# Kernel tuning notes

Measured on AMD Instinct MI355X. Metric: run time of the kernel, lower is better.

Reference implementation:

```python
import jax, jax.numpy as jnp
import numpy as np

N_IND, N_ORG, N_EXT = 1_000_000, 300_000, 100_000
F = 64
E = 1_000_000
# (src_type, dst_type) per relation, in HeteroConv dict order:
# txn: ind->ind, org->ind, ext->ind, ind->org, org->org, ext->org; role: ind->org;
# rev_txn: ind->ind, org->ind, ext->ind, ind->org, org->org, ext->org; rev_role: org->ind
RELS = [("ind","ind"),("org","ind"),("ext","ind"),("ind","org"),("org","org"),("ext","org"),
        ("ind","org"),("ind","ind"),("org","ind"),("ext","ind"),("ind","org"),("org","org"),
        ("ext","org"),("org","ind")]
N_OF = {"ind": N_IND, "org": N_ORG, "ext": N_EXT}


def setup_inputs() -> dict:
    key = jax.random.key(0)
    ks = jax.random.split(key, 8)
    x_ind = jax.random.normal(ks[0], (N_IND, F), dtype=jnp.float32)
    x_org = jax.random.normal(ks[1], (N_ORG, F), dtype=jnp.float32)
    x_ext = jax.random.normal(ks[2], (N_EXT, F), dtype=jnp.float32)
    Wl = jax.random.normal(ks[3], (14, F, 1), dtype=jnp.float32) * 0.1
    Wr = jax.random.normal(ks[4], (14, F, 1), dtype=jnp.float32) * 0.1
    b = jax.random.normal(ks[5], (14, 1), dtype=jnp.float32) * 0.1
    # Per-relation edge_index with src/dst ids in the correct node-count ranges.
    eis = []
    for r, (s, d) in enumerate(RELS):
        k1, k2 = jax.random.split(jax.random.fold_in(ks[6], r))
        src = jax.random.randint(k1, (E,), 0, N_OF[s], dtype=jnp.int32)
        dst = jax.random.randint(k2, (E,), 0, N_OF[d], dtype=jnp.int32)
        eis.append(jnp.stack([src, dst]))
    edge_index = jnp.stack(eis)  # [14, 2, E]
    return {"x_ind": x_ind, "x_org": x_org, "x_ext": x_ext,
            "Wl": Wl, "Wr": Wr, "b": b, "edge_index": edge_index}


def _segment_mean(feat, dst, num_segments):
    # PyG 'mean' aggr: zero for isolated dst nodes.
    s = jax.ops.segment_sum(feat, dst, num_segments=num_segments)          # [N_dst, F]
    c = jax.ops.segment_sum(jnp.ones((dst.shape[0], 1), feat.dtype), dst,
                            num_segments=num_segments)                      # [N_dst, 1]
    return s / jnp.maximum(c, 1.0)


def reference(x_ind, x_org, x_ext, Wl, Wr, b, edge_index):
    x = {"ind": x_ind, "org": x_org, "ext": x_ext}
    out = {"ind": jnp.zeros((N_IND, 1), x_ind.dtype),
           "org": jnp.zeros((N_ORG, 1), x_org.dtype)}
    for r, (s, d) in enumerate(RELS):
        src, dst = edge_index[r, 0], edge_index[r, 1]
        agg = _segment_mean(x[s][src], dst, N_OF[d])   # mean of neighbor feats [N_dst, F]
        # SAGEConv: lin_l(agg) + lin_r(x_dst); bias lives in lin_l. HeteroConv sums relations.
        out[d] = out[d] + agg @ Wl[r] + x[d] @ Wr[r] + b[r]
    pred_ind = jax.nn.sigmoid(out["ind"])[:, 0]
    pred_org = jax.nn.sigmoid(out["org"])[:, 0]
    return (pred_ind, pred_org)
```

## Files before the change

kernel.cpp:

```cpp
#include <hip/hip_runtime.h>
#include <hip/hip_fp16.h>

#define N_IND 1000000
#define N_ORG 300000
#define N_EXT 100000
#define F 64
#define E_PER 1000000
#define NREL 14

#define BW 1024
#define NB_IND 977
#define NB_ORG 293
#define NBKT 1270
#define NB_H 1024
#define CHUNK 8192
#define COLS_PER_REL 123
#define NCOL (NREL * COLS_PER_REL)
#define LAST_N (E_PER - (COLS_PER_REL - 1) * CHUNK)
#define COLS_PER_TYPE (7 * COLS_PER_REL)
#define TSCAT 512

#define FIX_SCALE 262144.0f
#define FIX_INV   3.814697265625e-6f

static const size_t OFF_PAY      = 0;
static const size_t OFF_CNTOFF   = 14106624;
static const size_t OFF_CNTOFF_T = 15869952;
static const size_t OFF_P_IND    = 17633280;
static const size_t OFF_P_ORG    = 20133280;
static const size_t OFF_P_EXT    = 20883280;
static const size_t OFF_BASE_IND = 21083280;
static const size_t OFF_BASE_ORG = 22083280;
static const size_t OFF_WM_IND   = 22383280;
static const size_t OFF_WM_ORG   = 22383664;
static const size_t OFF_WM_EXT   = 22384048;
static const size_t OFF_BSUM     = 22384304;

__global__ void prep_kernel(const float* __restrict__ Wl,
                            const float* __restrict__ Wr,
                            const float* __restrict__ b,
                            float* __restrict__ wm_ind,
                            float* __restrict__ wm_org,
                            float* __restrict__ wm_ext,
                            float* __restrict__ bsum) {
    int t = threadIdx.x;
    const int ind_wl[5] = {0, 3, 6, 7, 10};
    const int org_wl[5] = {1, 4, 8, 11, 13};
    const int ext_wl[4] = {2, 5, 9, 12};
    const int ind_r[7]  = {0, 1, 2, 7, 8, 9, 13};
    const int org_r[7]  = {3, 4, 5, 6, 10, 11, 12};
#pragma unroll
    for (int k = 0; k < 5; ++k) wm_ind[k * 64 + t] = Wl[ind_wl[k] * 64 + t];
#pragma unroll
    for (int k = 0; k < 5; ++k) wm_org[k * 64 + t] = Wl[org_wl[k] * 64 + t];
#pragma unroll
    for (int k = 0; k < 4; ++k) wm_ext[k * 64 + t] = Wl[ext_wl[k] * 64 + t];
    float si = 0.f, so = 0.f;
#pragma unroll
    for (int k = 0; k < 7; ++k) {
        si += Wr[ind_r[k] * 64 + t];
        so += Wr[org_r[k] * 64 + t];
    }
    wm_ind[5 * 64 + t] = si;
    wm_org[5 * 64 + t] = so;
    if (t == 0) {
        float bi = 0.f, bo = 0.f;
#pragma unroll
        for (int k = 0; k < 7; ++k) { bi += b[ind_r[k]]; bo += b[org_r[k]]; }
        bsum[0] = bi;
        bsum[1] = bo;
    }
}

template <int K, bool HASBASE>
__global__ __launch_bounds__(256) void proj_kernel(
    const float* __restrict__ x, int n,
    const float* __restrict__ wm,
    __half* __restrict__ p,
    float* __restrict__ base_out,
    const float* __restrict__ bsum) {
    int i = blockIdx.x * 256 + threadIdx.x;
    if (i >= n) return;
    const float4* xv = (const float4*)(x + (size_t)i * F);
    float acc[K];
#pragma unroll
    for (int k = 0; k < K; ++k) acc[k] = 0.f;
#pragma unroll
    for (int c = 0; c < 16; ++c) {
        float4 v = xv[c];
#pragma unroll
        for (int k = 0; k < K; ++k) {
            const float* w = wm + k * 64 + c * 4;
            acc[k] += v.x * w[0] + v.y * w[1] + v.z * w[2] + v.w * w[3];
        }
    }
    constexpr int NP = HASBASE ? K - 1 : K;
#pragma unroll
    for (int k = 0; k < NP; ++k) p[(size_t)k * n + i] = __float2half_rn(acc[k]);
    if (HASBASE) base_out[i] = acc[K - 1] + bsum[0];
}

__global__ __launch_bounds__(TSCAT, 8) void scatter_kernel(
    const int* __restrict__ ei,
    const unsigned short* __restrict__ p_ind,
    const unsigned short* __restrict__ p_org,
    const unsigned short* __restrict__ p_ext,
    unsigned* __restrict__ pay,
    unsigned* __restrict__ cntoff) {
    const int srcType[NREL] = {0,1,2,0,1,2,0,0,1,2,0,1,2,1};
    const int srcSlot[NREL] = {0,0,0,1,1,1,2,3,2,2,4,3,3,4};
    const int dstSlot[NREL] = {0,1,2,0,1,2,3,3,4,5,4,5,6,6};

    __shared__ unsigned h[NB_H];
    __shared__ unsigned stage[CHUNK];
    __shared__ unsigned wsum[8];

    const int t = threadIdx.x;
    const int lane = t & 63, wv = t >> 6;

    const int cid = blockIdx.x;
    const int r = cid / COLS_PER_REL;
    const int i = cid - r * COLS_PER_REL;
    const int n = (i == COLS_PER_REL - 1) ? LAST_N : CHUNK;
    const int n4 = n >> 2;
    const int* srcp = ei + ((size_t)r * 2 + 0) * E_PER + (size_t)i * CHUNK;
    const int* dstp = ei + ((size_t)r * 2 + 1) * E_PER + (size_t)i * CHUNK;
    const unsigned slotbits = (unsigned)dstSlot[r] << 10;
    const int st = srcType[r];
    const unsigned short* psrc =
        (st == 0) ? p_ind + (size_t)srcSlot[r] * N_IND :
        (st == 1) ? p_org + (size_t)srcSlot[r] * N_ORG :
                    p_ext + (size_t)srcSlot[r] * N_EXT;

    h[t * 2 + 0] = 0u;
    h[t * 2 + 1] = 0u;
    __syncthreads();
    const int4* dst4 = (const int4*)dstp;
    int4 dreg[4];
#pragma unroll
    for (int u = 0; u < 4; ++u) {
        int k = t + u * TSCAT;
        if (k < n4) {
            int4 d = dst4[k];
            dreg[u] = d;
            atomicAdd(&h[d.x >> 10], 1u);
            atomicAdd(&h[d.y >> 10], 1u);
            atomicAdd(&h[d.z >> 10], 1u);
            atomicAdd(&h[d.w >> 10], 1u);
        }
    }
    __syncthreads();

    unsigned loc0 = h[t * 2 + 0], loc1 = h[t * 2 + 1];
    unsigned s0 = loc0 + loc1;
    unsigned x = s0;
#pragma unroll
    for (int d = 1; d < 64; d <<= 1) {
        unsigned v = __shfl_up(x, d, 64);
        if (lane >= d) x += v;
    }
    if (lane == 63) wsum[wv] = x;
    __syncthreads();
    unsigned base = x - s0;
    for (int j = 0; j < wv; ++j) base += wsum[j];
    unsigned* co = cntoff + (size_t)cid * NB_H;
    co[t * 2 + 0] = (base << 16) | loc0;
    h[t * 2 + 0] = base;
    base += loc0;
    co[t * 2 + 1] = (base << 16) | loc1;
    h[t * 2 + 1] = base;
    __syncthreads();

    const int4* src4 = (const int4*)srcp;
#pragma unroll
    for (int u = 0; u < 4; ++u) {
        int k = t + u * TSCAT;
        if (k < n4) {
            int4 s = src4[k];
            int4 d = dreg[u];
#pragma unroll
            for (int q = 0; q < 4; ++q) {
                int src = (q == 0) ? s.x : (q == 1) ? s.y : (q == 2) ? s.z : s.w;
                int dst = (q == 0) ? d.x : (q == 1) ? d.y : (q == 2) ? d.z : d.w;
                unsigned pvbits = psrc[src];
                unsigned word = (pvbits << 16) | slotbits | ((unsigned)dst & (BW - 1));
                unsigned pos = atomicAdd(&h[dst >> 10], 1u);
                stage[pos] = word;
            }
        }
    }
    __syncthreads();

    uint4* payc4 = (uint4*)(pay + (size_t)cid * CHUNK);
    const uint4* st4 = (const uint4*)stage;
    for (int k = t; k < n4; k += TSCAT) payc4[k] = st4[k];
}

__global__ __launch_bounds__(256) void transpose_kernel(
    const unsigned* __restrict__ in, unsigned* __restrict__ out) {
    __shared__ unsigned tb[32][33];
    const int c0 = blockIdx.x * 32;
    const int r0 = blockIdx.y * 32;
    const int tx = threadIdx.x & 31, ty = threadIdx.x >> 5;
#pragma unroll
    for (int j = 0; j < 32; j += 8) {
        int r = r0 + ty + j, c = c0 + tx;
        if (r < NCOL && c < NB_H) tb[ty + j][tx] = in[(size_t)r * NB_H + c];
    }
    __syncthreads();
#pragma unroll
    for (int j = 0; j < 32; j += 8) {
        int r = c0 + ty + j, c = r0 + tx;
        if (r < NB_H && c < NCOL) out[(size_t)r * NCOL + c] = tb[tx][ty + j];
    }
}

__global__ __launch_bounds__(256) void gather_kernel(
    const unsigned* __restrict__ pay,
    const unsigned* __restrict__ cntoffT,
    const float* __restrict__ base_ind,
    const float* __restrict__ base_org,
    float* __restrict__ out) {
    __shared__ unsigned acc[7 * BW];
    const int blk = blockIdx.x;
    const int t = threadIdx.x;
    for (int j = t; j < 7 * BW; j += 256) acc[j] = 0u;
    __syncthreads();

    const bool isOrg = blk < NB_ORG;
    const int b = isOrg ? blk : blk - NB_ORG;
    const int relsI[7] = {0, 1, 2, 7, 8, 9, 13};
    const int relsO[7] = {3, 4, 5, 6, 10, 11, 12};

    const unsigned* row = cntoffT + (size_t)b * NCOL;
    for (int j = t; j < COLS_PER_TYPE; j += 256) {
        int rl = j / COLS_PER_REL;
        int c = j - rl * COLS_PER_REL;
        int cid = (isOrg ? relsO[rl] : relsI[rl]) * COLS_PER_REL + c;
        unsigned co = row[cid];
        unsigned cnt = co & 0xffffu;
        if (!cnt) continue;
        const unsigned* seg = pay + (size_t)cid * CHUNK + (co >> 16);
        for (unsigned e = 0; e < cnt; ++e) {
            unsigned w = seg[e];
            unsigned short hs = (unsigned short)(w >> 16);
            __half hh;
            __builtin_memcpy(&hh, &hs, 2);
            float pv = __half2float(hh);
            int fixed = (int)rintf(pv * FIX_SCALE);
            unsigned contrib = (1u << 26) + (unsigned)fixed;
            atomicAdd(&acc[((w >> 10) & 7u) * BW + (w & (BW - 1))], contrib);
        }
    }
    __syncthreads();

    const int nn = isOrg ? N_ORG : N_IND;
    const float* basep = isOrg ? base_org : base_ind;
    float* outp = isOrg ? out + N_IND : out;
    for (int loc = t; loc < BW; loc += 256) {
        int g = b * BW + loc;
        if (g < nn) {
            float a = basep[g];
#pragma unroll
            for (int k = 0; k < 7; ++k) {
                unsigned w = acc[k * BW + loc];
                int s26 = ((int)(w << 6)) >> 6;
                unsigned c = (w - (unsigned)s26) >> 26;
                a += (float)s26 * FIX_INV / fmaxf((float)c, 1.0f);
            }
            outp[g] = 1.0f / (1.0f + __expf(-a));
        }
    }
}

extern "C" void kernel_launch(void* const* d_in, const int* in_sizes, int n_in,
                              void* d_out, int out_size, void* d_ws, size_t ws_size,
                              hipStream_t stream) {
    const float* x_ind = (const float*)d_in[0];
    const float* x_org = (const float*)d_in[1];
    const float* x_ext = (const float*)d_in[2];
    const float* Wl    = (const float*)d_in[3];
    const float* Wr    = (const float*)d_in[4];
    const float* b     = (const float*)d_in[5];
    const int*   ei    = (const int*)d_in[6];
    float* out = (float*)d_out;

    float* ws = (float*)d_ws;
    unsigned* pay      = (unsigned*)(ws + OFF_PAY);
    unsigned* cntoff   = (unsigned*)(ws + OFF_CNTOFF);
    unsigned* cntoffT  = (unsigned*)(ws + OFF_CNTOFF_T);
    __half* p_ind      = (__half*)(ws + OFF_P_IND);
    __half* p_org      = (__half*)(ws + OFF_P_ORG);
    __half* p_ext      = (__half*)(ws + OFF_P_EXT);
    float* base_ind    = ws + OFF_BASE_IND;
    float* base_org    = ws + OFF_BASE_ORG;
    float* wm_ind      = ws + OFF_WM_IND;
    float* wm_org      = ws + OFF_WM_ORG;
    float* wm_ext      = ws + OFF_WM_EXT;
    float* bsum        = ws + OFF_BSUM;

    prep_kernel<<<1, 64, 0, stream>>>(Wl, Wr, b, wm_ind, wm_org, wm_ext, bsum);

    proj_kernel<6, true><<<(N_IND + 255) / 256, 256, 0, stream>>>(
        x_ind, N_IND, wm_ind, p_ind, base_ind, bsum + 0);
    proj_kernel<6, true><<<(N_ORG + 255) / 256, 256, 0, stream>>>(
        x_org, N_ORG, wm_org, p_org, base_org, bsum + 1);
    proj_kernel<4, false><<<(N_EXT + 255) / 256, 256, 0, stream>>>(
        x_ext, N_EXT, wm_ext, p_ext, nullptr, bsum);

    scatter_kernel<<<NCOL, TSCAT, 0, stream>>>(
        ei, (const unsigned short*)p_ind, (const unsigned short*)p_org,
        (const unsigned short*)p_ext, pay, cntoff);

    dim3 tgrid(NB_H / 32, (NCOL + 31) / 32);
    transpose_kernel<<<tgrid, 256, 0, stream>>>(cntoff, cntoffT);

    gather_kernel<<<NBKT, 256, 0, stream>>>(pay, cntoffT, base_ind, base_org, out);
}
```

Before: 265.9 us.

## Double scatter chunk size, widen blocks, and vectorize gather payload reads

Result: no change. 263.2 us (-1.0%).

```diff
diff --git a/kernel.cpp b/kernel.cpp
--- a/kernel.cpp
+++ b/kernel.cpp
@@ -13,28 +13,28 @@
 #define NB_ORG 293
 #define NBKT 1270
 #define NB_H 1024
-#define CHUNK 8192
-#define COLS_PER_REL 123
+#define CHUNK 16384
+#define COLS_PER_REL 62
 #define NCOL (NREL * COLS_PER_REL)
 #define LAST_N (E_PER - (COLS_PER_REL - 1) * CHUNK)
 #define COLS_PER_TYPE (7 * COLS_PER_REL)
-#define TSCAT 512
+#define TSCAT 1024
 
 #define FIX_SCALE 262144.0f
 #define FIX_INV   3.814697265625e-6f
 
 static const size_t OFF_PAY      = 0;
-static const size_t OFF_CNTOFF   = 14106624;
-static const size_t OFF_CNTOFF_T = 15869952;
-static const size_t OFF_P_IND    = 17633280;
-static const size_t OFF_P_ORG    = 20133280;
-static const size_t OFF_P_EXT    = 20883280;
-static const size_t OFF_BASE_IND = 21083280;
-static const size_t OFF_BASE_ORG = 22083280;
-static const size_t OFF_WM_IND   = 22383280;
-static const size_t OFF_WM_ORG   = 22383664;
-static const size_t OFF_WM_EXT   = 22384048;
-static const size_t OFF_BSUM     = 22384304;
+static const size_t OFF_CNTOFF   = 14221312;
+static const size_t OFF_CNTOFF_T = 15110144;
+static const size_t OFF_P_IND    = 15998976;
+static const size_t OFF_P_ORG    = 18498976;
+static const size_t OFF_P_EXT    = 19248976;
+static const size_t OFF_BASE_IND = 19448976;
+static const size_t OFF_BASE_ORG = 20448976;
+static const size_t OFF_WM_IND   = 20748976;
+static const size_t OFF_WM_ORG   = 20749360;
+static const size_t OFF_WM_EXT   = 20749744;
+static const size_t OFF_BSUM     = 20750000;
 
 __global__ void prep_kernel(const float* __restrict__ Wl,
                             const float* __restrict__ Wr,
@@ -113,7 +113,7 @@
 
     __shared__ unsigned h[NB_H];
     __shared__ unsigned stage[CHUNK];
-    __shared__ unsigned wsum[8];
+    __shared__ unsigned wsum[16];
 
     const int t = threadIdx.x;
     const int lane = t & 63, wv = t >> 6;
@@ -132,8 +132,7 @@
         (st == 1) ? p_org + (size_t)srcSlot[r] * N_ORG :
                     p_ext + (size_t)srcSlot[r] * N_EXT;
 
-    h[t * 2 + 0] = 0u;
-    h[t * 2 + 1] = 0u;
+    h[t] = 0u;
     __syncthreads();
     const int4* dst4 = (const int4*)dstp;
     int4 dreg[4];
@@ -151,9 +150,8 @@
     }
     __syncthreads();
 
-    unsigned loc0 = h[t * 2 + 0], loc1 = h[t * 2 + 1];
-    unsigned s0 = loc0 + loc1;
-    unsigned x = s0;
+    unsigned loc0 = h[t];
+    unsigned x = loc0;
 #pragma unroll
     for (int d = 1; d < 64; d <<= 1) {
         unsigned v = __shfl_up(x, d, 64);
@@ -161,14 +159,11 @@
     }
     if (lane == 63) wsum[wv] = x;
     __syncthreads();
-    unsigned base = x - s0;
+    unsigned base = x - loc0;
     for (int j = 0; j < wv; ++j) base += wsum[j];
     unsigned* co = cntoff + (size_t)cid * NB_H;
-    co[t * 2 + 0] = (base << 16) | loc0;
-    h[t * 2 + 0] = base;
-    base += loc0;
-    co[t * 2 + 1] = (base << 16) | loc1;
-    h[t * 2 + 1] = base;
+    co[t] = (base << 16) | loc0;
+    h[t] = base;
     __syncthreads();
 
     const int4* src4 = (const int4*)srcp;
@@ -215,7 +210,7 @@
     }
 }
 
-__global__ __launch_bounds__(256) void gather_kernel(
+__global__ __launch_bounds__(512) void gather_kernel(
     const unsigned* __restrict__ pay,
     const unsigned* __restrict__ cntoffT,
     const float* __restrict__ base_ind,
@@ -224,7 +219,7 @@
     __shared__ unsigned acc[7 * BW];
     const int blk = blockIdx.x;
     const int t = threadIdx.x;
-    for (int j = t; j < 7 * BW; j += 256) acc[j] = 0u;
+    for (int j = t; j < 7 * BW; j += 512) acc[j] = 0u;
     __syncthreads();
 
     const bool isOrg = blk < NB_ORG;
@@ -232,8 +227,17 @@
     const int relsI[7] = {0, 1, 2, 7, 8, 9, 13};
     const int relsO[7] = {3, 4, 5, 6, 10, 11, 12};
 
+#define PROC(w) {                                                        \
+        unsigned short hs = (unsigned short)((w) >> 16);                 \
+        __half hh;                                                       \
+        __builtin_memcpy(&hh, &hs, 2);                                   \
+        float pv = __half2float(hh);                                     \
+        int fixed = (int)rintf(pv * FIX_SCALE);                          \
+        atomicAdd(&acc[(((w) >> 10) & 7u) * BW + ((w) & (BW - 1))],      \
+                  (1u << 26) + (unsigned)fixed); }
+
     const unsigned* row = cntoffT + (size_t)b * NCOL;
-    for (int j = t; j < COLS_PER_TYPE; j += 256) {
+    for (int j = t; j < COLS_PER_TYPE; j += 512) {
         int rl = j / COLS_PER_REL;
         int c = j - rl * COLS_PER_REL;
         int cid = (isOrg ? relsO[rl] : relsI[rl]) * COLS_PER_REL + c;
@@ -241,23 +245,25 @@
         unsigned cnt = co & 0xffffu;
         if (!cnt) continue;
         const unsigned* seg = pay + (size_t)cid * CHUNK + (co >> 16);
-        for (unsigned e = 0; e < cnt; ++e) {
-            unsigned w = seg[e];
-            unsigned short hs = (unsigned short)(w >> 16);
-            __half hh;
-            __builtin_memcpy(&hh, &hs, 2);
-            float pv = __half2float(hh);
-            int fixed = (int)rintf(pv * FIX_SCALE);
-            unsigned contrib = (1u << 26) + (unsigned)fixed;
-            atomicAdd(&acc[((w >> 10) & 7u) * BW + (w & (BW - 1))], contrib);
-        }
-    }
+        unsigned e = 0;
+        unsigned head = (4u - (((unsigned)(size_t)seg >> 2) & 3u)) & 3u;
+        if (head > cnt) head = cnt;
+        for (; e < head; ++e) PROC(seg[e]);
+        unsigned nq = (cnt - e) >> 2;
+        const uint4* seg4 = (const uint4*)(seg + e);
+        for (unsigned q = 0; q < nq; ++q) {
+            uint4 w4 = seg4[q];
+            PROC(w4.x); PROC(w4.y); PROC(w4.z); PROC(w4.w);
+        }
+        for (e += nq * 4; e < cnt; ++e) PROC(seg[e]);
+    }
+#undef PROC
     __syncthreads();
 
     const int nn = isOrg ? N_ORG : N_IND;
     const float* basep = isOrg ? base_org : base_ind;
     float* outp = isOrg ? out + N_IND : out;
-    for (int loc = t; loc < BW; loc += 256) {
+    for (int loc = t; loc < BW; loc += 512) {
         int g = b * BW + loc;
         if (g < nn) {
             float a = basep[g];
@@ -315,5 +321,5 @@
     dim3 tgrid(NB_H / 32, (NCOL + 31) / 32);
     transpose_kernel<<<tgrid, 256, 0, stream>>>(cntoff, cntoffT);
 
-    gather_kernel<<<NBKT, 256, 0, stream>>>(pay, cntoffT, base_ind, base_org, out);
-}
+    gather_kernel<<<NBKT, 512, 0, stream>>>(pay, cntoffT, base_ind, base_org, out);
+}
```
